# Kernel tuning notes

Hardware: AMD Instinct MI355X
Metric: run time of the kernel (lower is better)

## Reference

```python
import jax, jax.numpy as jnp
import numpy as np

HEADS = 8
DIM_HEAD = 64
SCALE = DIM_HEAD ** -0.5


def setup_inputs() -> dict:
    key = jax.random.key(0)
    ks = jax.random.split(key, 6)
    B, T, C, H, W = 16, 64, 512, 64, 64
    inner = HEADS * DIM_HEAD  # 512
    return {
        "vision_feature": jax.random.normal(ks[0], (B, C, H, W), jnp.float32),
        "language_feature": jax.random.normal(ks[1], (B, T, C), jnp.float32),
        "mask": jnp.ones((B, T), jnp.int32),  # unused by the module's forward
        "Wq": jax.random.normal(ks[2], (inner, C), jnp.float32) * (C ** -0.5),
        "Wk": jax.random.normal(ks[3], (inner, C), jnp.float32) * (C ** -0.5),
        "Wv": jax.random.normal(ks[4], (inner, C), jnp.float32) * (C ** -0.5),
        "Wo": jax.random.normal(ks[5], (C, inner), jnp.float32) * (inner ** -0.5),
    }


def reference(vision_feature, language_feature, mask, Wq, Wk, Wv, Wo):
    B, T, C = language_feature.shape
    _, _, H, W = vision_feature.shape
    S = H * W
    # 1x1 conv projections == matmuls over the channel dim
    q = jnp.einsum('btc,ic->bti', language_feature, Wq)           # (B, T, inner)
    vis = vision_feature.reshape(B, C, S)                          # (B, C, S)
    k = jnp.einsum('ic,bcs->bis', Wk, vis)                         # (B, inner, S)
    v = jnp.einsum('ic,bcs->bis', Wv, vis)                         # (B, inner, S)
    # split heads: channel index = n*dim_head + d  (n outermost)
    q = q.reshape(B, T, HEADS, DIM_HEAD).transpose(2, 0, 1, 3)     # (h, B, T, d)
    k = k.reshape(B, HEADS, DIM_HEAD, S).transpose(1, 0, 2, 3)     # (h, B, d, S)
    v = v.reshape(B, HEADS, DIM_HEAD, S).transpose(1, 0, 3, 2)     # (h, B, S, d)
    att = jax.nn.softmax(jnp.einsum('hbtd,hbds->hbts', q, k) * SCALE, axis=-1)
    out = jnp.einsum('hbts,hbsd->hbtd', att, v)                    # (h, B, T, d)
    # merge heads back: b (n c) tokens -> equivalently (B, T, h*d)
    out = out.transpose(1, 2, 0, 3).reshape(B, T, HEADS * DIM_HEAD)
    out = jnp.einsum('bti,oi->bto', out, Wo)                       # (B, T, C)
    return out
```

## Files before the change

### kernel.cpp

```cpp
#include <hip/hip_runtime.h>
#include <stdint.h>

typedef __attribute__((ext_vector_type(8))) short short8;
typedef __attribute__((ext_vector_type(4))) short short4v;
typedef __attribute__((ext_vector_type(4))) float float4v;
typedef __attribute__((ext_vector_type(2))) unsigned int uint2v;
typedef __attribute__((ext_vector_type(8))) __bf16 bf16x8;

#define NCH 4

__device__ __forceinline__ float4v mfma16x16x32(short8 a, short8 b, float4v c) {
  return __builtin_amdgcn_mfma_f32_16x16x32_bf16(
      __builtin_bit_cast(bf16x8, a), __builtin_bit_cast(bf16x8, b), c, 0, 0, 0);
}

__device__ __forceinline__ short f2bf(float f) {
  uint32_t u = __builtin_bit_cast(uint32_t, f);
  u += 0x7fffu + ((u >> 16) & 1u);
  return (short)(u >> 16);
}

__device__ __forceinline__ float bf2f(short s) {
  return __builtin_bit_cast(float, ((uint32_t)(uint16_t)s) << 16);
}

__device__ __forceinline__ uint32_t cvt_pk_bf16(float a, float b) {
  uint32_t r;
  asm("v_cvt_pk_bf16_f32 %0, %1, %2" : "=v"(r) : "v"(a), "v"(b));
  return r;
}

__device__ __forceinline__ void load_lds16(const short* g, short* l) {
  __builtin_amdgcn_global_load_lds(
      (const __attribute__((address_space(1))) void*)g,
      (__attribute__((address_space(3))) void*)l, 16, 0, 0);
}

__global__ __launch_bounds__(256) void convert5(
    const float* __restrict__ sl, short* __restrict__ dl,
    const float* __restrict__ s1, short* __restrict__ d1,
    const float* __restrict__ s2, short* __restrict__ d2,
    const float* __restrict__ s3, short* __restrict__ d3,
    const float* __restrict__ s4, short* __restrict__ d4) {
  const float* src; short* dst; int n4;
  switch (blockIdx.y) {
    case 0: src = sl; dst = dl; n4 = 131072; break;
    case 1: src = s1; dst = d1; n4 = 65536; break;
    case 2: src = s2; dst = d2; n4 = 65536; break;
    case 3: src = s3; dst = d3; n4 = 65536; break;
    default: src = s4; dst = d4; n4 = 65536; break;
  }
  const int stride = gridDim.x * blockDim.x;
  for (int i = blockIdx.x * blockDim.x + threadIdx.x; i < n4; i += stride) {
    float4v v = *(const float4v*)(src + (long)i * 4);
    short4v o;
#pragma unroll
    for (int r = 0; r < 4; r++) o[r] = f2bf(v[r]);
    *(short4v*)(dst + (long)i * 4) = o;
  }
}

template <int OUT_F32>
__global__ __launch_bounds__(256) void gemm_nt(
    const short* __restrict__ A, const short* __restrict__ B,
    void* __restrict__ C, int K, int ldc, float scale) {
  __shared__ alignas(16) short smem[24576];
  const int tid = threadIdx.x;
  const int lane = tid & 63, w = tid >> 6;
  const int quad = lane >> 4, l16 = lane & 15;
  const int wm = w >> 1, wn = w & 1;
  const long m0 = (long)blockIdx.y * 128, n0 = (long)blockIdx.x * 128;

  float4v acc[4][4];
#pragma unroll
  for (int i = 0; i < 4; i++)
#pragma unroll
    for (int j = 0; j < 4; j++) acc[i][j] = (float4v)0.0f;

  const int srow = tid >> 2;
  const int scol = (((tid & 3) ^ ((srow >> 1) & 3))) * 8;
  const int nit = K >> 5;

#define STAGE_NT(t, base)                                                       \
  do {                                                                          \
    load_lds16(&A[(m0 + srow) * K + (t) * 32 + scol], &smem[(base) + tid * 8]); \
    load_lds16(&A[(m0 + 64 + srow) * K + (t) * 32 + scol],                      \
               &smem[(base) + 2048 + tid * 8]);                                 \
    load_lds16(&B[(n0 + srow) * K + (t) * 32 + scol],                           \
               &smem[(base) + 4096 + tid * 8]);                                 \
    load_lds16(&B[(n0 + 64 + srow) * K + (t) * 32 + scol],                      \
               &smem[(base) + 6144 + tid * 8]);                                 \
  } while (0)

  STAGE_NT(0, 0);
  if (nit > 1) STAGE_NT(1, 8192);

  for (int it = 0; it < nit; ++it) {
    const int base = (it % 3) * 8192;
    if (it + 1 < nit) asm volatile("s_waitcnt vmcnt(4)" ::: "memory");
    else              asm volatile("s_waitcnt vmcnt(0)" ::: "memory");
    __builtin_amdgcn_s_barrier();

    if (it + 2 < nit) STAGE_NT(it + 2, ((it + 2) % 3) * 8192);

    const short* lA = &smem[base];
    const short* lB = &smem[base + 4096];
    short8 af[4], bf[4];
#pragma unroll
    for (int t = 0; t < 4; t++) {
      const int ra = wm * 64 + t * 16 + l16;
      const int rb = wn * 64 + t * 16 + l16;
      af[t] = *(const short8*)&lA[ra * 32 + ((quad ^ ((ra >> 1) & 3)) * 8)];
      bf[t] = *(const short8*)&lB[rb * 32 + ((quad ^ ((rb >> 1) & 3)) * 8)];
    }
    __builtin_amdgcn_s_setprio(1);
#pragma unroll
    for (int i = 0; i < 4; i++)
#pragma unroll
      for (int j = 0; j < 4; j++)
        acc[i][j] = mfma16x16x32(af[i], bf[j], acc[i][j]);
    __builtin_amdgcn_s_setprio(0);
  }
#undef STAGE_NT

  const int cm = wm * 64 + quad * 4;
  const int cn = wn * 64 + l16;
  if (OUT_F32) {
    float* Cf = (float*)C;
#pragma unroll
    for (int i = 0; i < 4; i++)
#pragma unroll
      for (int j = 0; j < 4; j++) {
        const long gn = n0 + cn + j * 16;
#pragma unroll
        for (int r = 0; r < 4; r++)
          Cf[(m0 + cm + i * 16 + r) * (long)ldc + gn] = acc[i][j][r] * scale;
      }
  } else {
    short* Cs = (short*)C;
#pragma unroll
    for (int i = 0; i < 4; i++)
#pragma unroll
      for (int j = 0; j < 4; j++) {
        const long gn = n0 + cn + j * 16;
#pragma unroll
        for (int r = 0; r < 4; r++)
          Cs[(m0 + cm + i * 16 + r) * (long)ldc + gn] = f2bf(acc[i][j][r] * scale);
      }
  }
}

__global__ __launch_bounds__(512, 4) void gemm_kv(
    const short* __restrict__ Wk, const short* __restrict__ Wv,
    const short* __restrict__ visT, long sV,
    short* __restrict__ kout, short* __restrict__ vout, long sKV) {
  __shared__ alignas(16) short smem[36864];
  const int tid = threadIdx.x;
  const int lane = tid & 63, w = tid >> 6;
  const int quad = lane >> 4, l16 = lane & 15;
  const int role = w >> 2;
  const int wq = w & 3, wm = wq >> 1, wn = wq & 1;
  const long n0 = (long)blockIdx.x * 128;
  const long m0 = (long)blockIdx.y * 128;
  const short* vis = visT + blockIdx.z * sV;
  short* kz = kout + blockIdx.z * sKV;
  short* vz = vout + blockIdx.z * sKV;

  float4v acc[4][4];
#pragma unroll
  for (int i = 0; i < 4; i++)
#pragma unroll
    for (int j = 0; j < 4; j++) acc[i][j] = (float4v)0.0f;

  const int srow = tid >> 2;
  const int scol = (((tid & 3) ^ ((srow >> 1) & 3))) * 8;

  const short* gWk = &Wk[(m0 + srow) * 512 + scol];
  const short* gWv = &Wv[(m0 + srow) * 512 + scol];
  const short* gV = &vis[(n0 + srow) * 512 + scol];

#define STAGE_KV(t, base)                                      \
  do {                                                         \
    load_lds16(gWk + (t) * 32, &smem[(base) + tid * 8]);       \
    load_lds16(gWv + (t) * 32, &smem[(base) + 4096 + tid * 8]);\
    load_lds16(gV + (t) * 32, &smem[(base) + 8192 + tid * 8]); \
  } while (0)

  STAGE_KV(0, 0);
  STAGE_KV(1, 12288);

  for (int it = 0; it < 16; ++it) {
    const int base = (it % 3) * 12288;
    if (it < 15) asm volatile("s_waitcnt vmcnt(3)" ::: "memory");
    else         asm volatile("s_waitcnt vmcnt(0)" ::: "memory");
    __builtin_amdgcn_s_barrier();

    if (it + 2 < 16) STAGE_KV(it + 2, ((it + 2) % 3) * 12288);

    const short* lW = &smem[base + (role ? 4096 : 0)];
    const short* lVis = &smem[base + 8192];
    short8 af[4], bf[4];
#pragma unroll
    for (int t = 0; t < 4; t++) {
      const int ra = wm * 64 + t * 16 + l16;
      const int rb = wn * 64 + t * 16 + l16;
      af[t] = *(const short8*)&lW[ra * 32 + ((quad ^ ((ra >> 1) & 3)) * 8)];
      bf[t] = *(const short8*)&lVis[rb * 32 + ((quad ^ ((rb >> 1) & 3)) * 8)];
    }
    __builtin_amdgcn_s_setprio(1);
#pragma unroll
    for (int i = 0; i < 4; i++)
#pragma unroll
      for (int j = 0; j < 4; j++)
        acc[i][j] = mfma16x16x32(af[i], bf[j], acc[i][j]);
    __builtin_amdgcn_s_setprio(0);
  }
#undef STAGE_KV

  const int cm = wm * 64 + quad * 4;
  const int cn = wn * 64 + l16;

  if (role == 1) {
#pragma unroll
    for (int i = 0; i < 4; i++)
#pragma unroll
      for (int j = 0; j < 4; j++) {
        const long gn = n0 + cn + j * 16;
#pragma unroll
        for (int r = 0; r < 4; r++)
          vz[(m0 + cm + i * 16 + r) * 4096 + gn] = f2bf(acc[i][j][r]);
      }
  }

  short* scratch = smem;
#pragma unroll
  for (int h = 0; h < 2; h++) {
    __syncthreads();
    if (role == 0 && wn == h) {
#pragma unroll
      for (int j = 0; j < 4; j++)
#pragma unroll
        for (int i = 0; i < 4; i++) {
          const int nloc = j * 16 + l16;
          const int m = wm * 64 + i * 16 + quad * 4;
          short4v pk;
#pragma unroll
          for (int r = 0; r < 4; r++) pk[r] = f2bf(acc[i][j][r]);
          *(short4v*)&scratch[nloc * 136 + m] = pk;
        }
    }
    __syncthreads();
    {
      const int row = tid >> 3;
      const int off = (tid & 7) * 16;
      short8 v0 = *(const short8*)&scratch[row * 136 + off];
      short8 v1 = *(const short8*)&scratch[row * 136 + off + 8];
      *(short8*)&kz[(n0 + h * 64 + row) * 512 + m0 + off] = v0;
      *(short8*)&kz[(n0 + h * 64 + row) * 512 + m0 + off + 8] = v1;
    }
  }
}

__global__ __launch_bounds__(256) void transpose_f2b(
    const float* __restrict__ vis, short* __restrict__ visT) {
  __shared__ alignas(16) short buf[64][68];
  const int tid = threadIdx.x;
  const long bz = blockIdx.z;
  const long s0 = (long)blockIdx.x * 64;
  const long c0 = (long)blockIdx.y * 64;
  const float* src = vis + bz * 512 * 4096;
  short* dst = visT + bz * 4096 * 512;
  const int tr = tid >> 4;
  const int tc4 = (tid & 15) * 4;
#pragma unroll
  for (int i = 0; i < 4; i++) {
    const int c = tr + i * 16;
    float4v val = *(const float4v*)&src[(c0 + c) * 4096 + s0 + tc4];
    buf[tc4 + 0][c] = f2bf(val[0]);
    buf[tc4 + 1][c] = f2bf(val[1]);
    buf[tc4 + 2][c] = f2bf(val[2]);
    buf[tc4 + 3][c] = f2bf(val[3]);
  }
  __syncthreads();
#pragma unroll
  for (int i = 0; i < 4; i++) {
    const int s = tr + i * 16;
    short4v val = *(const short4v*)&buf[s][tc4];
    *(short4v*)&dst[(s0 + s) * 512 + c0 + tc4] = val;
  }
}

__global__ __launch_bounds__(256) void attn_part(
    const short* __restrict__ q, const short* __restrict__ kws,
    const short* __restrict__ vws, float* __restrict__ Opart,
    float* __restrict__ lpart, int b0) {
  const int h = blockIdx.x;
  const int bz = blockIdx.y;
  const int ch = blockIdx.z;
  const int tid = threadIdx.x;
  const int lane = tid & 63, w = tid >> 6;
  const int quad = lane >> 4, l16 = lane & 15;

  __shared__ alignas(16) short lq[64 * 64];
  __shared__ alignas(16) short lk[128 * 64];
  __shared__ alignas(16) short lv[64 * 128];
  __shared__ alignas(16) short lp[64 * 128];
  __shared__ float lsum[64];

  const short* qb = q + ((long)(b0 + bz) * 64) * 512 + h * 64;
  const short* kb = kws + (long)bz * 4096 * 512 + h * 64;
  const short* vb = vws + (long)bz * 512 * 4096 + (long)h * 64 * 4096;

  if (tid < 64) lsum[tid] = 0.0f;
  {
    const int qr = tid >> 3;
    const int qc = ((tid & 7) ^ (qr & 7)) * 8;
    load_lds16(&qb[qr * 512 + qc], &lq[tid * 8]);
    load_lds16(&qb[(32 + qr) * 512 + qc], &lq[2048 + tid * 8]);
  }
  const int s0_first = ch * (4096 / NCH);
  const int send = s0_first + (4096 / NCH);
#pragma unroll
  for (int it = 0; it < 4; it++) {
    const int li = tid + it * 256;
    const int kr = li >> 3;
    const int kc = ((li & 7) ^ (kr & 7)) * 8;
    load_lds16(&kb[(long)(s0_first + kr) * 512 + kc], &lk[li * 8]);
  }
#pragma unroll
  for (int it = 0; it < 4; it++) {
    const int li = tid + it * 256;
    const int vr = li >> 4;
    const int vc = ((li & 15) ^ (vr & 7)) * 8;
    load_lds16(&vb[(long)vr * 4096 + s0_first + vc], &lv[li * 8]);
  }
  __syncthreads();

  short8 aq[4][2];
#pragma unroll
  for (int mt = 0; mt < 4; mt++)
#pragma unroll
    for (int ks = 0; ks < 2; ks++) {
      const int ra = mt * 16 + l16;
      aq[mt][ks] = *(const short8*)&lq[ra * 64 + (((ks * 4 + quad) ^ (ra & 7)) * 8)];
    }

  float4v osc[4];
#pragma unroll
  for (int mt = 0; mt < 4; mt++) osc[mt] = (float4v)0.0f;
  float lrow[4] = {0.0f, 0.0f, 0.0f, 0.0f};

  const int cbase = w * 4 + (quad >> 1);
  const int sub = (quad & 1) * 4;

  for (int s0 = s0_first; s0 < send; s0 += 128) {
    short8 bk[2][2];
#pragma unroll
    for (int ks = 0; ks < 2; ks++)
#pragma unroll
      for (int si = 0; si < 2; si++) {
        const int rb = (2 * w + si) * 16 + l16;
        bk[ks][si] = *(const short8*)&lk[rb * 64 + (((ks * 4 + quad) ^ (rb & 7)) * 8)];
      }
    short8 bv[4];
#pragma unroll
    for (int ks = 0; ks < 4; ks++) {
      const int rv = w * 16 + l16;
      bv[ks] = *(const short8*)&lv[rv * 128 + (((ks * 4 + quad) ^ (rv & 7)) * 8)];
    }
    __syncthreads();

    if (s0 + 128 < send) {
#pragma unroll
      for (int it = 0; it < 4; it++) {
        const int li = tid + it * 256;
        const int kr = li >> 3;
        const int kc = ((li & 7) ^ (kr & 7)) * 8;
        load_lds16(&kb[(long)(s0 + 128 + kr) * 512 + kc], &lk[li * 8]);
      }
#pragma unroll
      for (int it = 0; it < 4; it++) {
        const int li = tid + it * 256;
        const int vr = li >> 4;
        const int vc = ((li & 15) ^ (vr & 7)) * 8;
        load_lds16(&vb[(long)vr * 4096 + s0 + 128 + vc], &lv[li * 8]);
      }
    }

    float4v sc[2][4];
#pragma unroll
    for (int si = 0; si < 2; si++)
#pragma unroll
      for (int tj = 0; tj < 4; tj++) sc[si][tj] = (float4v)0.0f;
#pragma unroll
    for (int ks = 0; ks < 2; ks++)
#pragma unroll
      for (int si = 0; si < 2; si++)
#pragma unroll
        for (int tj = 0; tj < 4; tj++)
          sc[si][tj] = mfma16x16x32(bk[ks][si], aq[tj][ks], sc[si][tj]);

#pragma unroll
    for (int si = 0; si < 2; si++) {
      const int c = cbase + si * 2;
#pragma unroll
      for (int tj = 0; tj < 4; tj++) {
        float p0 = __expf(fminf(fmaxf(sc[si][tj][0], -80.0f), 30.0f));
        float p1 = __expf(fminf(fmaxf(sc[si][tj][1], -80.0f), 30.0f));
        float p2 = __expf(fminf(fmaxf(sc[si][tj][2], -80.0f), 30.0f));
        float p3 = __expf(fminf(fmaxf(sc[si][tj][3], -80.0f), 30.0f));
        const uint32_t u01 = cvt_pk_bf16(p0, p1);
        const uint32_t u23 = cvt_pk_bf16(p2, p3);
        lrow[tj] += __builtin_bit_cast(float, u01 << 16) +
                    __builtin_bit_cast(float, u01 & 0xffff0000u) +
                    __builtin_bit_cast(float, u23 << 16) +
                    __builtin_bit_cast(float, u23 & 0xffff0000u);
        const int t = tj * 16 + l16;
        uint2v val; val.x = u01; val.y = u23;
        *(uint2v*)&lp[t * 128 + ((c ^ (t & 7)) * 8) + sub] = val;
      }
    }
    asm volatile("s_waitcnt lgkmcnt(0)" ::: "memory");
    __builtin_amdgcn_sched_barrier(0);
    __builtin_amdgcn_s_barrier();

#pragma unroll
    for (int ks = 0; ks < 4; ks++)
#pragma unroll
      for (int mt = 0; mt < 4; mt++) {
        const int rp = mt * 16 + l16;
        const short8 ap = *(const short8*)&lp[rp * 128 + (((ks * 4 + quad) ^ (rp & 7)) * 8)];
        osc[mt] = mfma16x16x32(ap, bv[ks], osc[mt]);
      }
    __syncthreads();
  }

#pragma unroll
  for (int tj = 0; tj < 4; tj++) {
    float v = lrow[tj];
    v += __shfl_xor(v, 16);
    v += __shfl_xor(v, 32);
    if (quad == 0) atomicAdd(&lsum[tj * 16 + l16], v);
  }
  __syncthreads();

  const long bh = bz * 8 + h;
  float* op = Opart + ((bh * NCH + ch) * 64) * 64 + w * 16 + l16;
#pragma unroll
  for (int mt = 0; mt < 4; mt++)
#pragma unroll
    for (int r = 0; r < 4; r++)
      op[(long)(mt * 16 + quad * 4 + r) * 64] = osc[mt][r];
  if (tid < 64) lpart[(bh * NCH + ch) * 64 + tid] = lsum[tid];
}

__global__ __launch_bounds__(256) void attn_combine(
    const float* __restrict__ Opart, const float* __restrict__ lpart,
    short* __restrict__ tmp, int b0, int nbh) {
  const int total4 = nbh * 1024;
  for (int i4 = blockIdx.x * 256 + threadIdx.x; i4 < total4;
       i4 += gridDim.x * 256) {
    const int bh = i4 >> 10;
    const int td = (i4 & 1023) << 2;
    const int t = td >> 6;
    float4v o = (float4v)0.0f;
    float l = 0.0f;
#pragma unroll
    for (int c = 0; c < NCH; c++) {
      o += *(const float4v*)&Opart[(((long)bh * NCH + c) << 12) + td];
      l += lpart[(bh * NCH + c) * 64 + t];
    }
    const float inv = 1.0f / l;
    const int b = b0 + (bh >> 3), h = bh & 7;
    short4v r;
#pragma unroll
    for (int j = 0; j < 4; j++) r[j] = f2bf(o[j] * inv);
    *(short4v*)&tmp[((long)b * 64 + t) * 512 + h * 64 + (td & 63)] = r;
  }
}

extern "C" void kernel_launch(void* const* d_in, const int* in_sizes, int n_in,
                              void* d_out, int out_size, void* d_ws, size_t ws_size,
                              hipStream_t stream) {
  (void)in_sizes; (void)n_in; (void)out_size;
  const float* vis = (const float*)d_in[0];
  const float* lang = (const float*)d_in[1];
  const float* Wq = (const float*)d_in[3];
  const float* Wk = (const float*)d_in[4];
  const float* Wv = (const float*)d_in[5];
  const float* Wo = (const float*)d_in[6];
  float* out = (float*)d_out;

  char* ws = (char*)d_ws;
  const size_t MB = 1 << 20;
  short* q_ws = (short*)(ws + 0 * MB);
  short* tmp_ws = (short*)(ws + 1 * MB);
  short* langb = (short*)(ws + 2 * MB);
  short* Wqb = (short*)(ws + 3 * MB);
  short* Wkb = (short*)(ws + 3 * MB + 512 * 1024);
  short* Wvb = (short*)(ws + 4 * MB);
  short* Wob = (short*)(ws + 4 * MB + 512 * 1024);
  char* grp = ws + 5 * MB;

  const long batch_elems = 4096l * 512;
  int g = 16;
  const int cands[5] = {1, 2, 4, 8, 16};
  for (int ci = 0; ci < 5; ci++) {
    const size_t need = 5 * MB + 3ull * (16 / cands[ci]) * batch_elems * 2;
    if (need <= ws_size) { g = cands[ci]; break; }
  }
  const int Bg = 16 / g;
  short* visT = (short*)grp;
  short* k_ws = visT + (long)Bg * batch_elems;
  short* v_ws = k_ws + (long)Bg * batch_elems;
  float* Opart = (float*)visT;
  float* lptr = Opart + (long)Bg * 8 * NCH * 4096;

  convert5<<<dim3(128, 5), 256, 0, stream>>>(lang, langb, Wq, Wqb, Wk, Wkb,
                                             Wv, Wvb, Wo, Wob);

  gemm_nt<0><<<dim3(4, 8), 256, 0, stream>>>(langb, Wqb, q_ws, 512, 512, 0.125f);

  for (int gi = 0; gi < g; gi++) {
    const int b0 = gi * Bg;
    transpose_f2b<<<dim3(64, 8, Bg), 256, 0, stream>>>(vis + (long)b0 * batch_elems, visT);
    gemm_kv<<<dim3(32, 4, Bg), 512, 0, stream>>>(Wkb, Wvb, visT, batch_elems,
                                                 k_ws, v_ws, batch_elems);
    attn_part<<<dim3(8, Bg, NCH), 256, 0, stream>>>(q_ws, k_ws, v_ws, Opart, lptr, b0);
    attn_combine<<<512, 256, 0, stream>>>(Opart, lptr, tmp_ws, b0, Bg * 8);
  }

  gemm_nt<1><<<dim3(4, 8), 256, 0, stream>>>(tmp_ws, Wob, out, 512, 512, 1.0f);
}
```

Baseline: 331.5 us.

## Fuse vision fp32-to-bf16 transpose into the K/V projection GEMM load path

Removes the separate transpose_f2b kernel. gemm_kv now reads fp32 vision features directly from global memory, converts them to packed bf16 in registers and writes them swizzled into LDS, with the register loads software-pipelined alongside the async weight loads. This drops the extra write and re-read of a bf16 transposed copy and one kernel launch per group. The cost is that each K/V tile block now reads twice as many bytes of vision data as fp32 with scalar strided loads, and converts inline. Workspace layout and sizing are adjusted so Opart no longer aliases the removed visT buffer.

```diff
diff --git a/kernel.cpp b/kernel.cpp
--- a/kernel.cpp
+++ b/kernel.cpp
@@ -5,6 +5,7 @@
 typedef __attribute__((ext_vector_type(4))) short short4v;
 typedef __attribute__((ext_vector_type(4))) float float4v;
 typedef __attribute__((ext_vector_type(2))) unsigned int uint2v;
+typedef __attribute__((ext_vector_type(4))) unsigned int uint4v;
 typedef __attribute__((ext_vector_type(8))) __bf16 bf16x8;
 
 #define NCH 4
@@ -152,7 +153,7 @@
 
 __global__ __launch_bounds__(512, 4) void gemm_kv(
     const short* __restrict__ Wk, const short* __restrict__ Wv,
-    const short* __restrict__ visT, long sV,
+    const float* __restrict__ visf, long sV,
     short* __restrict__ kout, short* __restrict__ vout, long sKV) {
   __shared__ alignas(16) short smem[36864];
   const int tid = threadIdx.x;
@@ -162,7 +163,7 @@
   const int wq = w & 3, wm = wq >> 1, wn = wq & 1;
   const long n0 = (long)blockIdx.x * 128;
   const long m0 = (long)blockIdx.y * 128;
-  const short* vis = visT + blockIdx.z * sV;
+  const float* vis = visf + blockIdx.z * sV;
   short* kz = kout + blockIdx.z * sKV;
   short* vz = vout + blockIdx.z * sKV;
 
@@ -174,28 +175,59 @@
 
   const int srow = tid >> 2;
   const int scol = (((tid & 3) ^ ((srow >> 1) & 3))) * 8;
-
   const short* gWk = &Wk[(m0 + srow) * 512 + scol];
   const short* gWv = &Wv[(m0 + srow) * 512 + scol];
-  const short* gV = &vis[(n0 + srow) * 512 + scol];
-
-#define STAGE_KV(t, base)                                      \
-  do {                                                         \
-    load_lds16(gWk + (t) * 32, &smem[(base) + tid * 8]);       \
-    load_lds16(gWv + (t) * 32, &smem[(base) + 4096 + tid * 8]);\
-    load_lds16(gV + (t) * 32, &smem[(base) + 8192 + tid * 8]); \
+
+  const int sl = tid & 127;
+  const int oct = tid >> 7;
+  const float* gv = vis + (long)(oct * 8) * 4096 + n0 + sl;
+  const int woff = 8192 + sl * 32 + ((oct ^ ((sl >> 1) & 3)) * 8);
+
+#define STAGE_W(t, base)                                          \
+  do {                                                            \
+    load_lds16(gWk + (t) * 32, &smem[(base) + tid * 8]);          \
+    load_lds16(gWv + (t) * 32, &smem[(base) + 4096 + tid * 8]);   \
   } while (0)
 
-  STAGE_KV(0, 0);
-  STAGE_KV(1, 12288);
+#define VLOAD(t)                                                  \
+  do {                                                            \
+    _Pragma("unroll")                                             \
+    for (int j = 0; j < 8; j++)                                   \
+      vf[j] = gv[((t) * 32 + j) * 4096];                          \
+  } while (0)
+
+#define VWRITE(base)                                              \
+  do {                                                            \
+    uint4v pw;                                                    \
+    pw.x = cvt_pk_bf16(vf[0], vf[1]);                             \
+    pw.y = cvt_pk_bf16(vf[2], vf[3]);                             \
+    pw.z = cvt_pk_bf16(vf[4], vf[5]);                             \
+    pw.w = cvt_pk_bf16(vf[6], vf[7]);                             \
+    *(uint4v*)&smem[(base) + woff] = pw;                          \
+  } while (0)
+
+  float vf[8];
+  VLOAD(0);
+  asm volatile("s_waitcnt vmcnt(0)" ::: "memory");
+  VWRITE(0);
+  VLOAD(1);
+  __builtin_amdgcn_sched_barrier(0);
+  STAGE_W(0, 0);
+  STAGE_W(1, 12288);
 
   for (int it = 0; it < 16; ++it) {
     const int base = (it % 3) * 12288;
-    if (it < 15) asm volatile("s_waitcnt vmcnt(3)" ::: "memory");
+    if (it < 15) asm volatile("s_waitcnt vmcnt(2)" ::: "memory");
     else         asm volatile("s_waitcnt vmcnt(0)" ::: "memory");
+    if (it < 15) VWRITE(((it + 1) % 3) * 12288);
+    asm volatile("s_waitcnt lgkmcnt(0)" ::: "memory");
     __builtin_amdgcn_s_barrier();
 
-    if (it + 2 < 16) STAGE_KV(it + 2, ((it + 2) % 3) * 12288);
+    if (it + 2 < 16) {
+      VLOAD(it + 2);
+      __builtin_amdgcn_sched_barrier(0);
+      STAGE_W(it + 2, ((it + 2) % 3) * 12288);
+    }
 
     const short* lW = &smem[base + (role ? 4096 : 0)];
     const short* lVis = &smem[base + 8192];
@@ -215,7 +247,9 @@
         acc[i][j] = mfma16x16x32(af[i], bf[j], acc[i][j]);
     __builtin_amdgcn_s_setprio(0);
   }
-#undef STAGE_KV
+#undef STAGE_W
+#undef VLOAD
+#undef VWRITE
 
   const int cm = wm * 64 + quad * 4;
   const int cn = wn * 64 + l16;
@@ -258,35 +292,6 @@
       *(short8*)&kz[(n0 + h * 64 + row) * 512 + m0 + off] = v0;
       *(short8*)&kz[(n0 + h * 64 + row) * 512 + m0 + off + 8] = v1;
     }
-  }
-}
-
-__global__ __launch_bounds__(256) void transpose_f2b(
-    const float* __restrict__ vis, short* __restrict__ visT) {
-  __shared__ alignas(16) short buf[64][68];
-  const int tid = threadIdx.x;
-  const long bz = blockIdx.z;
-  const long s0 = (long)blockIdx.x * 64;
-  const long c0 = (long)blockIdx.y * 64;
-  const float* src = vis + bz * 512 * 4096;
-  short* dst = visT + bz * 4096 * 512;
-  const int tr = tid >> 4;
-  const int tc4 = (tid & 15) * 4;
-#pragma unroll
-  for (int i = 0; i < 4; i++) {
-    const int c = tr + i * 16;
-    float4v val = *(const float4v*)&src[(c0 + c) * 4096 + s0 + tc4];
-    buf[tc4 + 0][c] = f2bf(val[0]);
-    buf[tc4 + 1][c] = f2bf(val[1]);
-    buf[tc4 + 2][c] = f2bf(val[2]);
-    buf[tc4 + 3][c] = f2bf(val[3]);
-  }
-  __syncthreads();
-#pragma unroll
-  for (int i = 0; i < 4; i++) {
-    const int s = tr + i * 16;
-    short4v val = *(const short4v*)&buf[s][tc4];
-    *(short4v*)&dst[(s0 + s) * 512 + c0 + tc4] = val;
   }
 }
 
@@ -503,17 +508,20 @@
   char* grp = ws + 5 * MB;
 
   const long batch_elems = 4096l * 512;
+  const long vis_f32 = 512l * 4096;
   int g = 16;
   const int cands[5] = {1, 2, 4, 8, 16};
   for (int ci = 0; ci < 5; ci++) {
-    const size_t need = 5 * MB + 3ull * (16 / cands[ci]) * batch_elems * 2;
+    const int Bgc = 16 / cands[ci];
+    const size_t need = 5 * MB + 2ull * Bgc * batch_elems * 2
+                        + (size_t)Bgc * 8 * NCH * 4096 * 4
+                        + (size_t)Bgc * 8 * NCH * 64 * 4 + 4096;
     if (need <= ws_size) { g = cands[ci]; break; }
   }
   const int Bg = 16 / g;
-  short* visT = (short*)grp;
-  short* k_ws = visT + (long)Bg * batch_elems;
+  short* k_ws = (short*)grp;
   short* v_ws = k_ws + (long)Bg * batch_elems;
-  float* Opart = (float*)visT;
+  float* Opart = (float*)(v_ws + (long)Bg * batch_elems);
   float* lptr = Opart + (long)Bg * 8 * NCH * 4096;
 
   convert5<<<dim3(128, 5), 256, 0, stream>>>(lang, langb, Wq, Wqb, Wk, Wkb,
@@ -523,9 +531,8 @@
 
   for (int gi = 0; gi < g; gi++) {
     const int b0 = gi * Bg;
-    transpose_f2b<<<dim3(64, 8, Bg), 256, 0, stream>>>(vis + (long)b0 * batch_elems, visT);
-    gemm_kv<<<dim3(32, 4, Bg), 512, 0, stream>>>(Wkb, Wvb, visT, batch_elems,
-                                                 k_ws, v_ws, batch_elems);
+    gemm_kv<<<dim3(32, 4, Bg), 512, 0, stream>>>(Wkb, Wvb, vis + (long)b0 * vis_f32,
+                                                 vis_f32, k_ws, v_ws, batch_elems);
     attn_part<<<dim3(8, Bg, NCH), 256, 0, stream>>>(q_ws, k_ws, v_ws, Opart, lptr, b0);
     attn_combine<<<512, 256, 0, stream>>>(Opart, lptr, tmp_ws, b0, Bg * 8);
   }
```

Result: no change. 327.9 us (-1.1%).
